# Kernel optimization log

Measured on AMD Instinct MI355X. Metric: run time of the kernel, lower is better.

Reference implementation:

```python
import jax, jax.numpy as jnp
import numpy as np

B, S, H = 4, 4096, 768
NB = 16            # n_blocks (first factor)
BSZ = H // NB      # 48, block size
LN_EPS = 1e-12


def setup_inputs() -> dict:
    key = jax.random.key(0)
    ks = jax.random.split(key, 6)
    hidden_states = jax.random.normal(ks[0], (B, S, H), dtype=jnp.float32)
    # Monarch factors: B1 has NB blocks of (BSZ,BSZ); B2 has BSZ blocks of (NB,NB)
    w1_blocks = jax.random.normal(ks[1], (NB, BSZ, BSZ), dtype=jnp.float32) / np.sqrt(BSZ)
    w2_blocks = jax.random.normal(ks[2], (BSZ, NB, NB), dtype=jnp.float32) / np.sqrt(NB)
    gate_w = jax.random.normal(ks[3], (H, H), dtype=jnp.float32) / np.sqrt(H)
    gate_b = jnp.zeros((H,), dtype=jnp.float32)
    out_w = jax.random.normal(ks[4], (H, H), dtype=jnp.float32) / np.sqrt(H)
    out_b = jnp.zeros((H,), dtype=jnp.float32)
    ln_gamma = jnp.ones((H,), dtype=jnp.float32)
    ln_beta = jnp.zeros((H,), dtype=jnp.float32)
    return {
        "hidden_states": hidden_states,
        "w1_blocks": w1_blocks,
        "w2_blocks": w2_blocks,
        "gate_w": gate_w,
        "gate_b": gate_b,
        "out_w": out_w,
        "out_b": out_b,
        "ln_gamma": ln_gamma,
        "ln_beta": ln_beta,
    }


def _monarch(x, w1, w2):
    # x: [B, S, H]; Monarch product P B2 P B1 applied to last dim.
    b, s, h = x.shape
    y = x.reshape(b, s, NB, BSZ)
    y = jnp.einsum('bski,kij->bskj', y, w1)      # block-diag (NB blocks of BSZxBSZ)
    y = jnp.swapaxes(y, -1, -2)                  # permute: [B,S,BSZ,NB]
    y = jnp.einsum('bsqi,qij->bsqj', y, w2)      # block-diag (BSZ blocks of NBxNB)
    y = jnp.swapaxes(y, -1, -2)                  # permute back: [B,S,NB,BSZ]
    return y.reshape(b, s, h)


def _layernorm(x, gamma, beta, eps):
    mu = jnp.mean(x, axis=-1, keepdims=True)
    var = jnp.mean(jnp.square(x - mu), axis=-1, keepdims=True)
    return (x - mu) * jax.lax.rsqrt(var + eps) * gamma + beta


def reference(hidden_states, w1_blocks, w2_blocks, gate_w, gate_b,
              out_w, out_b, ln_gamma, ln_beta):
    residual = hidden_states
    mixed = _monarch(hidden_states, w1_blocks, w2_blocks)
    gate = jax.nn.sigmoid(hidden_states @ gate_w.T + gate_b)
    h = mixed * gate
    h = h @ out_w.T + out_b
    # dropout is identity in eval / p=0
    return _layernorm(h + residual, ln_gamma, ln_beta, LN_EPS)
```

## Files before the change

kernel.cpp:

```cpp
#include <hip/hip_runtime.h>
#include <hip/hip_bf16.h>
#include <stdint.h>

#define HD 768

typedef __attribute__((ext_vector_type(8))) short bf16x8;
typedef __attribute__((ext_vector_type(4))) float f32x4;

typedef __attribute__((address_space(3))) void lds_void_t;
typedef const __attribute__((address_space(1))) void gbl_void_t;

__device__ inline void gload_lds16(const void* g, void* l) {
  __builtin_amdgcn_global_load_lds((gbl_void_t*)g, (lds_void_t*)l, 16, 0, 0);
}

__device__ inline unsigned short f2bf(float f) {
  union { float f; unsigned int u; } v; v.f = f;
  return (unsigned short)((v.u + 0x7fffu + ((v.u >> 16) & 1u)) >> 16);
}
__device__ inline float bf2f(unsigned short u) {
  union { unsigned int uu; float f; } v; v.uu = ((unsigned int)u) << 16;
  return v.f;
}

#define BAR() asm volatile("s_barrier" ::: "memory")
#define LGKM(N) { asm volatile("s_waitcnt lgkmcnt(" #N ")" ::: "memory"); __builtin_amdgcn_sched_barrier(0); }
#define VMC(N) asm volatile("s_waitcnt vmcnt(" #N ")" ::: "memory")

__global__ void prep_all_kernel(const float* __restrict__ x,
                                const float* __restrict__ gw, const float* __restrict__ ow,
                                const float* __restrict__ w1, const float* __restrict__ w2,
                                unsigned short* __restrict__ xb,
                                unsigned short* __restrict__ Gwb, unsigned short* __restrict__ Lwb,
                                unsigned short* __restrict__ Opk) {
  int bid = blockIdx.x;
  if (bid < 12288) {
    int i = bid * 256 + threadIdx.x;
    float4 v = ((const float4*)x)[i];
    ushort4 o;
    o.x = f2bf(v.x); o.y = f2bf(v.y); o.z = f2bf(v.z); o.w = f2bf(v.w);
    ((ushort4*)xb)[i] = o;
  } else if (bid < 14592) {
    int e = (bid - 12288) * 256 + threadIdx.x;
    Gwb[e] = f2bf(gw[e]);
  } else if (bid < 16896) {
    int e = (bid - 14592) * 256 + threadIdx.x;
    int n = e / 768, m = e - (e / 768) * 768;
    int k = n / 48, q = n - k * 48;
    int i2 = m / 48, ii = m - i2 * 48;
    float v = w1[(i2 * 48 + ii) * 48 + q] * w2[(q * 16 + i2) * 16 + k];
    Lwb[e] = f2bf(v);
  } else {
    int r = (bid - 16896) * 256 + threadIdx.x;
    int lane = r & 63;
    int ks = (r >> 6) % 24;
    int nt = r / (24 * 64);
    int n = nt * 16 + (lane & 15);
    int k = ks * 32 + (lane >> 4) * 8;
    bf16x8 pack;
#pragma unroll
    for (int j = 0; j < 8; ++j) pack[j] = (short)f2bf(ow[(size_t)n * HD + k + j]);
    *(bf16x8*)(Opk + (size_t)r * 8) = pack;
  }
}

__global__ __launch_bounds__(256, 2)
void gatemix_kernel(const unsigned short* __restrict__ xb,
                    const unsigned short* __restrict__ Gwb,
                    const unsigned short* __restrict__ Lwb,
                    const float* __restrict__ gate_b,
                    unsigned short* __restrict__ hb) {
  __shared__ __align__(16) unsigned char lds[81920];
  const int tid = threadIdx.x, lane = tid & 63;
  const int wid = tid >> 6, wm = wid >> 1, wn = wid & 1;
  const int lr = lane & 15, lg = lane >> 4;

  const int b = blockIdx.x;
  const int work = (b & 7) * 128 + (b >> 3);
  const int panel = work >> 3, nwin = work & 7;
  const size_t m0 = (size_t)panel * 128;
  const int n0 = nwin * 96;

  const int r0 = tid >> 3;
  const int sw = ((tid & 7) << 4) ^ ((r0 & 7) << 4);
  const int v0 = (0 * 32 + r0) * 1536 + sw;
  const int v1 = (1 * 32 + r0) * 1536 + sw;
  const int v2 = (2 * 32 + r0) * 1536 + sw;
  const int v3 = (3 * 32 + r0) * 1536 + sw;
  const unsigned char* aS = (const unsigned char*)xb + m0 * 1536;
  const unsigned char* gS = (const unsigned char*)Gwb + (size_t)n0 * 1536;
  const unsigned char* lS = (const unsigned char*)Lwb + (size_t)n0 * 1536;

#define STAGE_A(KT, BUF) { const unsigned char* s = aS + (KT) * 128; \
    gload_lds16(s + v0, lds + (BUF) * 16384 + tid * 16); \
    gload_lds16(s + v1, lds + (BUF) * 16384 + 4096 + tid * 16); \
    gload_lds16(s + v2, lds + (BUF) * 16384 + 8192 + tid * 16); \
    gload_lds16(s + v3, lds + (BUF) * 16384 + 12288 + tid * 16); }
#define STAGE_BG(KT, BUF) { const unsigned char* s = gS + (KT) * 128; \
    gload_lds16(s + v0, lds + 32768 + (BUF) * 12288 + tid * 16); \
    gload_lds16(s + v1, lds + 32768 + (BUF) * 12288 + 4096 + tid * 16); \
    gload_lds16(s + v2, lds + 32768 + (BUF) * 12288 + 8192 + tid * 16); }
#define STAGE_BL(KT, BUF) { const unsigned char* s = lS + (KT) * 128; \
    gload_lds16(s + v0, lds + 57344 + (BUF) * 12288 + tid * 16); \
    gload_lds16(s + v1, lds + 57344 + (BUF) * 12288 + 4096 + tid * 16); \
    gload_lds16(s + v2, lds + 57344 + (BUF) * 12288 + 8192 + tid * 16); }

  const int sx0 = (lg * 16) ^ ((lr & 7) << 4);
  const int sx1 = sx0 ^ 64;
  const unsigned char* baA0 = lds + (wm * 64 + lr) * 128 + sx0;
  const unsigned char* baA1 = lds + (wm * 64 + lr) * 128 + sx1;
  const unsigned char* baG0 = lds + 32768 + (wn * 48 + lr) * 128 + sx0;
  const unsigned char* baG1 = lds + 32768 + (wn * 48 + lr) * 128 + sx1;
  const unsigned char* baL0 = lds + 57344 + (wn * 48 + lr) * 128 + sx0;
  const unsigned char* baL1 = lds + 57344 + (wn * 48 + lr) * 128 + sx1;

  f32x4 accg[4][3], accm[4][3];
#pragma unroll
  for (int mt = 0; mt < 4; ++mt)
#pragma unroll
    for (int nt = 0; nt < 3; ++nt) { accg[mt][nt] = (f32x4){0,0,0,0}; accm[mt][nt] = (f32x4){0,0,0,0}; }

  bf16x8 aA[4], aB[4];
  bf16x8 bG[3], bL[3];

#define RD_AA(BUF) { _Pragma("unroll") for (int mt = 0; mt < 4; ++mt) \
      aA[mt] = *(const bf16x8*)(baA0 + (BUF) * 16384 + mt * 2048); }
#define RD_AB(BUF) { _Pragma("unroll") for (int mt = 0; mt < 4; ++mt) \
      aB[mt] = *(const bf16x8*)(baA1 + (BUF) * 16384 + mt * 2048); }
#define RD_BG0(BUF) { _Pragma("unroll") for (int nt = 0; nt < 3; ++nt) \
      bG[nt] = *(const bf16x8*)(baG0 + (BUF) * 12288 + nt * 2048); }
#define RD_BG1(BUF) { _Pragma("unroll") for (int nt = 0; nt < 3; ++nt) \
      bG[nt] = *(const bf16x8*)(baG1 + (BUF) * 12288 + nt * 2048); }
#define RD_BL0(BUF) { _Pragma("unroll") for (int nt = 0; nt < 3; ++nt) \
      bL[nt] = *(const bf16x8*)(baL0 + (BUF) * 12288 + nt * 2048); }
#define RD_BL1(BUF) { _Pragma("unroll") for (int nt = 0; nt < 3; ++nt) \
      bL[nt] = *(const bf16x8*)(baL1 + (BUF) * 12288 + nt * 2048); }
#define MM(ACC, AR, BR) { __builtin_amdgcn_s_setprio(1); \
    _Pragma("unroll") for (int mt = 0; mt < 4; ++mt) \
    _Pragma("unroll") for (int nt = 0; nt < 3; ++nt) \
      ACC[mt][nt] = __builtin_amdgcn_mfma_f32_16x16x32_bf16(AR[mt], BR[nt], ACC[mt][nt], 0, 0, 0); \
    __builtin_amdgcn_s_setprio(0); }

#define KT_BODY(KT, BUF, STG, VN) { \
    STAGE_BL((KT) + 1, (BUF) ^ 1); \
    RD_BL0(BUF); \
    LGKM(3); MM(accg, aA, bG); \
    RD_AB(BUF); RD_BG1(BUF); \
    LGKM(7); MM(accm, aA, bL); \
    RD_BL1(BUF); \
    LGKM(3); MM(accg, aB, bG); \
    BAR(); \
    if (STG) { STAGE_A((KT) + 2, BUF); STAGE_BG((KT) + 2, BUF); } \
    VMC(VN); \
    BAR(); \
    RD_AA((BUF) ^ 1); RD_BG0((BUF) ^ 1); \
    LGKM(7); MM(accm, aB, bL); }

  STAGE_A(0, 0); STAGE_BG(0, 0); STAGE_BL(0, 0); STAGE_A(1, 1); STAGE_BG(1, 1);
  VMC(7);
  BAR();
  RD_AA(0); RD_BG0(0);

#pragma unroll 1
  for (int kt = 0; kt < 10; kt += 2) {
    KT_BODY(kt, 0, 1, 7);
    KT_BODY(kt + 1, 1, 1, 7);
  }
  KT_BODY(10, 0, 0, 0);
  RD_BL0(1); LGKM(3); MM(accg, aA, bG);
  RD_AB(1); RD_BG1(1); LGKM(7); MM(accm, aA, bL);
  RD_BL1(1); LGKM(3); MM(accg, aB, bG);
  LGKM(0); MM(accm, aB, bL);

#pragma unroll
  for (int nt = 0; nt < 3; ++nt) {
    const int col = n0 + wn * 48 + nt * 16 + lr;
    const float gbv = gate_b[col];
#pragma unroll
    for (int mt = 0; mt < 4; ++mt) {
#pragma unroll
      for (int i = 0; i < 4; ++i) {
        float g = accg[mt][nt][i] + gbv;
        float s = 1.0f / (1.0f + __expf(-g));
        size_t row = m0 + wm * 64 + mt * 16 + lg * 4 + i;
        hb[row * 768 + col] = f2bf(s * accm[mt][nt][i]);
      }
    }
  }
#undef STAGE_A
#undef STAGE_BG
#undef STAGE_BL
#undef RD_AA
#undef RD_AB
#undef RD_BG0
#undef RD_BG1
#undef RD_BL0
#undef RD_BL1
#undef MM
#undef KT_BODY
}

__global__ __launch_bounds__(512, 2)
void out_ln_kernel(const unsigned short* __restrict__ hb,
                   const unsigned short* __restrict__ Opk,
                   const float* __restrict__ out_b,
                   const unsigned short* __restrict__ xb,
                   const float* __restrict__ gamma,
                   const float* __restrict__ beta,
                   float* __restrict__ out) {
  __shared__ __align__(16) unsigned char lds[16384];
  __shared__ float psum[64][8];
  __shared__ float psq[64][8];

  const int tid = threadIdx.x, lane = tid & 63, wid = tid >> 6;
  const int lr = lane & 15, lg = lane >> 4;
  const size_t m0 = (size_t)blockIdx.x * 64;

  const int srow = tid >> 3;
  const unsigned char* aSrc = (const unsigned char*)hb + (m0 + srow) * 1536
                              + (((tid & 7) << 4) ^ ((srow & 7) << 4));
#define STAGE_A(KT, BUF) gload_lds16(aSrc + (KT) * 128, lds + (BUF) * 8192 + tid * 16)

  const unsigned short* bBase = Opk + ((size_t)(wid * 6) * 24 * 64 + lane) * 8;
#define LOAD_B(KT, BR) { _Pragma("unroll") for (int nt = 0; nt < 6; ++nt) { \
      BR[nt * 2 + 0] = *(const bf16x8*)(bBase + nt * 12288 + ((KT) * 2 + 0) * 512); \
      BR[nt * 2 + 1] = *(const bf16x8*)(bBase + nt * 12288 + ((KT) * 2 + 1) * 512); } }

  const int sx0 = (lg * 16) ^ ((lr & 7) << 4);
  const unsigned char* baA0 = lds + lr * 128 + sx0;
  const unsigned char* baA1 = lds + lr * 128 + (sx0 ^ 64);
#define RD_A(BUF) { _Pragma("unroll") for (int mt = 0; mt < 4; ++mt) { \
      aF0[mt] = *(const bf16x8*)(baA0 + (BUF) * 8192 + mt * 2048); \
      aF1[mt] = *(const bf16x8*)(baA1 + (BUF) * 8192 + mt * 2048); } }

#define MM48(BR) { __builtin_amdgcn_s_setprio(1); \
    _Pragma("unroll") for (int mt = 0; mt < 4; ++mt) \
    _Pragma("unroll") for (int nt = 0; nt < 6; ++nt) { \
      acc[mt][nt] = __builtin_amdgcn_mfma_f32_16x16x32_bf16(aF0[mt], BR[nt * 2 + 0], acc[mt][nt], 0, 0, 0); \
      acc[mt][nt] = __builtin_amdgcn_mfma_f32_16x16x32_bf16(aF1[mt], BR[nt * 2 + 1], acc[mt][nt], 0, 0, 0); } \
    __builtin_amdgcn_s_setprio(0); }

  f32x4 acc[4][6];
#pragma unroll
  for (int mt = 0; mt < 4; ++mt)
#pragma unroll
    for (int nt = 0; nt < 6; ++nt) acc[mt][nt] = (f32x4){0, 0, 0, 0};

  bf16x8 aF0[4], aF1[4];
  bf16x8 bP[12], bQ[12];

#define KT_BODY(KT, BUF, BCUR, BNXT, LAST) { \
    if (!(LAST)) { STAGE_A((KT) + 1, (BUF) ^ 1); LOAD_B((KT) + 1, BNXT); } \
    RD_A(BUF); \
    LGKM(0); \
    if (!(LAST)) { VMC(13); } else { VMC(0); } \
    MM48(BCUR); \
    if (!(LAST)) { VMC(12); BAR(); } }

  STAGE_A(0, 0);
  LOAD_B(0, bP);
  VMC(12);
  BAR();

#pragma unroll 1
  for (int kt = 0; kt < 10; kt += 2) {
    KT_BODY(kt, 0, bP, bQ, 0);
    KT_BODY(kt + 1, 1, bQ, bP, 0);
  }
  KT_BODY(10, 0, bP, bQ, 0);
  KT_BODY(11, 1, bQ, bP, 1);

#pragma unroll
  for (int nt = 0; nt < 6; ++nt) {
    const int col = wid * 96 + nt * 16 + lr;
    const float obv = out_b[col];
#pragma unroll
    for (int mt = 0; mt < 4; ++mt) {
#pragma unroll
      for (int i = 0; i < 4; ++i) {
        size_t row = m0 + mt * 16 + lg * 4 + i;
        acc[mt][nt][i] += obv + bf2f(xb[row * 768 + col]);
      }
    }
  }
#pragma unroll
  for (int mt = 0; mt < 4; ++mt) {
#pragma unroll
    for (int i = 0; i < 4; ++i) {
      float s = 0.f, q = 0.f;
#pragma unroll
      for (int nt = 0; nt < 6; ++nt) { float v = acc[mt][nt][i]; s += v; q += v * v; }
#pragma unroll
      for (int off = 8; off >= 1; off >>= 1) {
        s += __shfl_xor(s, off);
        q += __shfl_xor(q, off);
      }
      if (lr == 0) {
        int rl = mt * 16 + lg * 4 + i;
        psum[rl][wid] = s; psq[rl][wid] = q;
      }
    }
  }
  __syncthreads();
#pragma unroll
  for (int mt = 0; mt < 4; ++mt) {
#pragma unroll
    for (int i = 0; i < 4; ++i) {
      int rl = mt * 16 + lg * 4 + i;
      float s = 0.f, q = 0.f;
#pragma unroll
      for (int w = 0; w < 8; ++w) { s += psum[rl][w]; q += psq[rl][w]; }
      float mu = s * (1.0f / 768.0f);
      float var = q * (1.0f / 768.0f) - mu * mu;
      var = var < 0.f ? 0.f : var;
      float rstd = rsqrtf(var + 1e-12f);
      size_t grow = m0 + rl;
#pragma unroll
      for (int nt = 0; nt < 6; ++nt) {
        int col = wid * 96 + nt * 16 + lr;
        out[grow * 768 + col] = (acc[mt][nt][i] - mu) * rstd * gamma[col] + beta[col];
      }
    }
  }
#undef STAGE_A
#undef LOAD_B
#undef RD_A
#undef MM48
#undef KT_BODY
}

extern "C" void kernel_launch(void* const* d_in, const int* in_sizes, int n_in,
                              void* d_out, int out_size, void* d_ws, size_t ws_size,
                              hipStream_t stream) {
  const float* x   = (const float*)d_in[0];
  const float* w1  = (const float*)d_in[1];
  const float* w2  = (const float*)d_in[2];
  const float* gw  = (const float*)d_in[3];
  const float* gb  = (const float*)d_in[4];
  const float* ow  = (const float*)d_in[5];
  const float* ob  = (const float*)d_in[6];
  const float* gam = (const float*)d_in[7];
  const float* bet = (const float*)d_in[8];
  float* out = (float*)d_out;

  char* ws = (char*)d_ws;
  unsigned short* xb  = (unsigned short*)(ws);
  unsigned short* hb  = (unsigned short*)(ws + 25165824);
  unsigned short* Gwb = (unsigned short*)(ws + 50331648);
  unsigned short* Lwb = (unsigned short*)(ws + 51511296);
  unsigned short* Opk = (unsigned short*)(ws + 52690944);

  prep_all_kernel<<<17184, 256, 0, stream>>>(x, gw, ow, w1, w2, xb, Gwb, Lwb, Opk);
  gatemix_kernel<<<1024, 256, 0, stream>>>(xb, Gwb, Lwb, gb, hb);
  out_ln_kernel<<<256, 512, 0, stream>>>(hb, Opk, ob, xb, gam, bet, out);
}
```

Before: 95.27 us.

## Fuse gate GEMM, factored Monarch mixing, out-proj and LayerNorm into one kernel

Replaces the three-kernel pipeline (x cast to bf16, a gate/Monarch GEMM writing an intermediate, then out-proj plus LayerNorm) with a small weight-prep kernel and a single fused kernel per 64-row tile. The fused kernel loads x once into LDS as bf16, runs the gate GEMM, applies the Monarch transform as two small block-diagonal MFMA stages through LDS scratch instead of a dense 768x768 product, writes the gated result back into the tile, then does the out-projection and LayerNorm. This removes the full-size bf16 x and h round-trips through global memory and about half the GEMM FLOPs. In exchange it uses about 150 KB of LDS per block with only 256 blocks, adds several barriers and serial phases, and the B operands come straight from global memory.

```diff
diff --git a/kernel.cpp b/kernel.cpp
--- a/kernel.cpp
+++ b/kernel.cpp
@@ -7,13 +7,6 @@
 typedef __attribute__((ext_vector_type(8))) short bf16x8;
 typedef __attribute__((ext_vector_type(4))) float f32x4;
 
-typedef __attribute__((address_space(3))) void lds_void_t;
-typedef const __attribute__((address_space(1))) void gbl_void_t;
-
-__device__ inline void gload_lds16(const void* g, void* l) {
-  __builtin_amdgcn_global_load_lds((gbl_void_t*)g, (lds_void_t*)l, 16, 0, 0);
-}
-
 __device__ inline unsigned short f2bf(float f) {
   union { float f; unsigned int u; } v; v.f = f;
   return (unsigned short)((v.u + 0x7fffu + ((v.u >> 16) & 1u)) >> 16);
@@ -23,35 +16,20 @@
   return v.f;
 }
 
-#define BAR() asm volatile("s_barrier" ::: "memory")
 #define LGKM(N) { asm volatile("s_waitcnt lgkmcnt(" #N ")" ::: "memory"); __builtin_amdgcn_sched_barrier(0); }
-#define VMC(N) asm volatile("s_waitcnt vmcnt(" #N ")" ::: "memory")
-
-__global__ void prep_all_kernel(const float* __restrict__ x,
-                                const float* __restrict__ gw, const float* __restrict__ ow,
-                                const float* __restrict__ w1, const float* __restrict__ w2,
-                                unsigned short* __restrict__ xb,
-                                unsigned short* __restrict__ Gwb, unsigned short* __restrict__ Lwb,
-                                unsigned short* __restrict__ Opk) {
+#define VMC(N) { asm volatile("s_waitcnt vmcnt(" #N ")" ::: "memory"); __builtin_amdgcn_sched_barrier(0); }
+
+__global__ void prep_kernel(const float* __restrict__ gw, const float* __restrict__ ow,
+                            const float* __restrict__ w1, const float* __restrict__ w2,
+                            unsigned short* __restrict__ Gpk,
+                            unsigned short* __restrict__ Opk,
+                            unsigned short* __restrict__ w1f,
+                            unsigned short* __restrict__ w2f) {
   int bid = blockIdx.x;
-  if (bid < 12288) {
-    int i = bid * 256 + threadIdx.x;
-    float4 v = ((const float4*)x)[i];
-    ushort4 o;
-    o.x = f2bf(v.x); o.y = f2bf(v.y); o.z = f2bf(v.z); o.w = f2bf(v.w);
-    ((ushort4*)xb)[i] = o;
-  } else if (bid < 14592) {
-    int e = (bid - 12288) * 256 + threadIdx.x;
-    Gwb[e] = f2bf(gw[e]);
-  } else if (bid < 16896) {
-    int e = (bid - 14592) * 256 + threadIdx.x;
-    int n = e / 768, m = e - (e / 768) * 768;
-    int k = n / 48, q = n - k * 48;
-    int i2 = m / 48, ii = m - i2 * 48;
-    float v = w1[(i2 * 48 + ii) * 48 + q] * w2[(q * 16 + i2) * 16 + k];
-    Lwb[e] = f2bf(v);
-  } else {
-    int r = (bid - 16896) * 256 + threadIdx.x;
+  if (bid < 576) {
+    const float* src = (bid < 288) ? gw : ow;
+    unsigned short* dst = (bid < 288) ? Gpk : Opk;
+    int r = ((bid < 288) ? bid : bid - 288) * 256 + threadIdx.x;
     int lane = r & 63;
     int ks = (r >> 6) % 24;
     int nt = r / (24 * 64);
@@ -59,156 +37,50 @@
     int k = ks * 32 + (lane >> 4) * 8;
     bf16x8 pack;
 #pragma unroll
-    for (int j = 0; j < 8; ++j) pack[j] = (short)f2bf(ow[(size_t)n * HD + k + j]);
-    *(bf16x8*)(Opk + (size_t)r * 8) = pack;
-  }
-}
-
-__global__ __launch_bounds__(256, 2)
-void gatemix_kernel(const unsigned short* __restrict__ xb,
-                    const unsigned short* __restrict__ Gwb,
-                    const unsigned short* __restrict__ Lwb,
-                    const float* __restrict__ gate_b,
-                    unsigned short* __restrict__ hb) {
-  __shared__ __align__(16) unsigned char lds[81920];
-  const int tid = threadIdx.x, lane = tid & 63;
-  const int wid = tid >> 6, wm = wid >> 1, wn = wid & 1;
-  const int lr = lane & 15, lg = lane >> 4;
-
-  const int b = blockIdx.x;
-  const int work = (b & 7) * 128 + (b >> 3);
-  const int panel = work >> 3, nwin = work & 7;
-  const size_t m0 = (size_t)panel * 128;
-  const int n0 = nwin * 96;
-
-  const int r0 = tid >> 3;
-  const int sw = ((tid & 7) << 4) ^ ((r0 & 7) << 4);
-  const int v0 = (0 * 32 + r0) * 1536 + sw;
-  const int v1 = (1 * 32 + r0) * 1536 + sw;
-  const int v2 = (2 * 32 + r0) * 1536 + sw;
-  const int v3 = (3 * 32 + r0) * 1536 + sw;
-  const unsigned char* aS = (const unsigned char*)xb + m0 * 1536;
-  const unsigned char* gS = (const unsigned char*)Gwb + (size_t)n0 * 1536;
-  const unsigned char* lS = (const unsigned char*)Lwb + (size_t)n0 * 1536;
-
-#define STAGE_A(KT, BUF) { const unsigned char* s = aS + (KT) * 128; \
-    gload_lds16(s + v0, lds + (BUF) * 16384 + tid * 16); \
-    gload_lds16(s + v1, lds + (BUF) * 16384 + 4096 + tid * 16); \
-    gload_lds16(s + v2, lds + (BUF) * 16384 + 8192 + tid * 16); \
-    gload_lds16(s + v3, lds + (BUF) * 16384 + 12288 + tid * 16); }
-#define STAGE_BG(KT, BUF) { const unsigned char* s = gS + (KT) * 128; \
-    gload_lds16(s + v0, lds + 32768 + (BUF) * 12288 + tid * 16); \
-    gload_lds16(s + v1, lds + 32768 + (BUF) * 12288 + 4096 + tid * 16); \
-    gload_lds16(s + v2, lds + 32768 + (BUF) * 12288 + 8192 + tid * 16); }
-#define STAGE_BL(KT, BUF) { const unsigned char* s = lS + (KT) * 128; \
-    gload_lds16(s + v0, lds + 57344 + (BUF) * 12288 + tid * 16); \
-    gload_lds16(s + v1, lds + 57344 + (BUF) * 12288 + 4096 + tid * 16); \
-    gload_lds16(s + v2, lds + 57344 + (BUF) * 12288 + 8192 + tid * 16); }
-
-  const int sx0 = (lg * 16) ^ ((lr & 7) << 4);
-  const int sx1 = sx0 ^ 64;
-  const unsigned char* baA0 = lds + (wm * 64 + lr) * 128 + sx0;
-  const unsigned char* baA1 = lds + (wm * 64 + lr) * 128 + sx1;
-  const unsigned char* baG0 = lds + 32768 + (wn * 48 + lr) * 128 + sx0;
-  const unsigned char* baG1 = lds + 32768 + (wn * 48 + lr) * 128 + sx1;
-  const unsigned char* baL0 = lds + 57344 + (wn * 48 + lr) * 128 + sx0;
-  const unsigned char* baL1 = lds + 57344 + (wn * 48 + lr) * 128 + sx1;
-
-  f32x4 accg[4][3], accm[4][3];
-#pragma unroll
-  for (int mt = 0; mt < 4; ++mt)
-#pragma unroll
-    for (int nt = 0; nt < 3; ++nt) { accg[mt][nt] = (f32x4){0,0,0,0}; accm[mt][nt] = (f32x4){0,0,0,0}; }
-
-  bf16x8 aA[4], aB[4];
-  bf16x8 bG[3], bL[3];
-
-#define RD_AA(BUF) { _Pragma("unroll") for (int mt = 0; mt < 4; ++mt) \
-      aA[mt] = *(const bf16x8*)(baA0 + (BUF) * 16384 + mt * 2048); }
-#define RD_AB(BUF) { _Pragma("unroll") for (int mt = 0; mt < 4; ++mt) \
-      aB[mt] = *(const bf16x8*)(baA1 + (BUF) * 16384 + mt * 2048); }
-#define RD_BG0(BUF) { _Pragma("unroll") for (int nt = 0; nt < 3; ++nt) \
-      bG[nt] = *(const bf16x8*)(baG0 + (BUF) * 12288 + nt * 2048); }
-#define RD_BG1(BUF) { _Pragma("unroll") for (int nt = 0; nt < 3; ++nt) \
-      bG[nt] = *(const bf16x8*)(baG1 + (BUF) * 12288 + nt * 2048); }
-#define RD_BL0(BUF) { _Pragma("unroll") for (int nt = 0; nt < 3; ++nt) \
-      bL[nt] = *(const bf16x8*)(baL0 + (BUF) * 12288 + nt * 2048); }
-#define RD_BL1(BUF) { _Pragma("unroll") for (int nt = 0; nt < 3; ++nt) \
-      bL[nt] = *(const bf16x8*)(baL1 + (BUF) * 12288 + nt * 2048); }
-#define MM(ACC, AR, BR) { __builtin_amdgcn_s_setprio(1); \
-    _Pragma("unroll") for (int mt = 0; mt < 4; ++mt) \
-    _Pragma("unroll") for (int nt = 0; nt < 3; ++nt) \
-      ACC[mt][nt] = __builtin_amdgcn_mfma_f32_16x16x32_bf16(AR[mt], BR[nt], ACC[mt][nt], 0, 0, 0); \
-    __builtin_amdgcn_s_setprio(0); }
-
-#define KT_BODY(KT, BUF, STG, VN) { \
-    STAGE_BL((KT) + 1, (BUF) ^ 1); \
-    RD_BL0(BUF); \
-    LGKM(3); MM(accg, aA, bG); \
-    RD_AB(BUF); RD_BG1(BUF); \
-    LGKM(7); MM(accm, aA, bL); \
-    RD_BL1(BUF); \
-    LGKM(3); MM(accg, aB, bG); \
-    BAR(); \
-    if (STG) { STAGE_A((KT) + 2, BUF); STAGE_BG((KT) + 2, BUF); } \
-    VMC(VN); \
-    BAR(); \
-    RD_AA((BUF) ^ 1); RD_BG0((BUF) ^ 1); \
-    LGKM(7); MM(accm, aB, bL); }
-
-  STAGE_A(0, 0); STAGE_BG(0, 0); STAGE_BL(0, 0); STAGE_A(1, 1); STAGE_BG(1, 1);
-  VMC(7);
-  BAR();
-  RD_AA(0); RD_BG0(0);
-
-#pragma unroll 1
-  for (int kt = 0; kt < 10; kt += 2) {
-    KT_BODY(kt, 0, 1, 7);
-    KT_BODY(kt + 1, 1, 1, 7);
-  }
-  KT_BODY(10, 0, 0, 0);
-  RD_BL0(1); LGKM(3); MM(accg, aA, bG);
-  RD_AB(1); RD_BG1(1); LGKM(7); MM(accm, aA, bL);
-  RD_BL1(1); LGKM(3); MM(accg, aB, bG);
-  LGKM(0); MM(accm, aB, bL);
-
-#pragma unroll
-  for (int nt = 0; nt < 3; ++nt) {
-    const int col = n0 + wn * 48 + nt * 16 + lr;
-    const float gbv = gate_b[col];
-#pragma unroll
-    for (int mt = 0; mt < 4; ++mt) {
-#pragma unroll
-      for (int i = 0; i < 4; ++i) {
-        float g = accg[mt][nt][i] + gbv;
-        float s = 1.0f / (1.0f + __expf(-g));
-        size_t row = m0 + wm * 64 + mt * 16 + lg * 4 + i;
-        hb[row * 768 + col] = f2bf(s * accm[mt][nt][i]);
-      }
-    }
-  }
-#undef STAGE_A
-#undef STAGE_BG
-#undef STAGE_BL
-#undef RD_AA
-#undef RD_AB
-#undef RD_BG0
-#undef RD_BG1
-#undef RD_BL0
-#undef RD_BL1
-#undef MM
-#undef KT_BODY
+    for (int j = 0; j < 8; ++j) pack[j] = (short)f2bf(src[(size_t)n * HD + k + j]);
+    *(bf16x8*)(dst + (size_t)r * 8) = pack;
+  } else if (bid < 600) {
+    int e = (bid - 576) * 256 + threadIdx.x;
+    int lane = e & 63, fi = e >> 6;
+    int ks = fi & 1, nt = (fi >> 1) % 3, k = fi / 6;
+    int lrr = lane & 15, lgg = lane >> 4;
+    int q = nt * 16 + lrr;
+    bf16x8 pack;
+#pragma unroll
+    for (int j = 0; j < 8; ++j) {
+      int kk = ks * 32 + lgg * 8 + j;
+      float v = (kk < 48) ? w1[(k * 48 + kk) * 48 + q] : 0.0f;
+      pack[j] = (short)f2bf(v);
+    }
+    *(bf16x8*)(w1f + (size_t)e * 8) = pack;
+  } else {
+    int e = (bid - 600) * 256 + threadIdx.x;
+    int lane = e & 63, q = e >> 6;
+    int lrr = lane & 15, lgg = lane >> 4;
+    bf16x8 pack;
+#pragma unroll
+    for (int j = 0; j < 8; ++j) {
+      int kk = lgg * 8 + j;
+      float v = (kk < 16) ? w2[(q * 16 + kk) * 16 + lrr] : 0.0f;
+      pack[j] = (short)f2bf(v);
+    }
+    *(bf16x8*)(w2f + (size_t)e * 8) = pack;
+  }
 }
 
 __global__ __launch_bounds__(512, 2)
-void out_ln_kernel(const unsigned short* __restrict__ hb,
-                   const unsigned short* __restrict__ Opk,
-                   const float* __restrict__ out_b,
-                   const unsigned short* __restrict__ xb,
-                   const float* __restrict__ gamma,
-                   const float* __restrict__ beta,
-                   float* __restrict__ out) {
-  __shared__ __align__(16) unsigned char lds[16384];
+void fused_kernel(const float* __restrict__ x,
+                  const unsigned short* __restrict__ Gpk,
+                  const unsigned short* __restrict__ Opk,
+                  const unsigned short* __restrict__ w1f,
+                  const unsigned short* __restrict__ w2f,
+                  const float* __restrict__ gate_b,
+                  const float* __restrict__ out_b,
+                  const float* __restrict__ gamma,
+                  const float* __restrict__ beta,
+                  float* __restrict__ out) {
+  __shared__ __align__(16) unsigned char tile[98304];
+  __shared__ __align__(16) unsigned char scratch[49152];
   __shared__ float psum[64][8];
   __shared__ float psq[64][8];
 
@@ -216,80 +88,152 @@
   const int lr = lane & 15, lg = lane >> 4;
   const size_t m0 = (size_t)blockIdx.x * 64;
 
-  const int srow = tid >> 3;
-  const unsigned char* aSrc = (const unsigned char*)hb + (m0 + srow) * 1536
-                              + (((tid & 7) << 4) ^ ((srow & 7) << 4));
-#define STAGE_A(KT, BUF) gload_lds16(aSrc + (KT) * 128, lds + (BUF) * 8192 + tid * 16)
-
-  const unsigned short* bBase = Opk + ((size_t)(wid * 6) * 24 * 64 + lane) * 8;
-#define LOAD_B(KT, BR) { _Pragma("unroll") for (int nt = 0; nt < 6; ++nt) { \
-      BR[nt * 2 + 0] = *(const bf16x8*)(bBase + nt * 12288 + ((KT) * 2 + 0) * 512); \
-      BR[nt * 2 + 1] = *(const bf16x8*)(bBase + nt * 12288 + ((KT) * 2 + 1) * 512); } }
+  float gbv[6], obv[6];
+#pragma unroll
+  for (int nt = 0; nt < 6; ++nt) {
+    int col = wid * 96 + nt * 16 + lr;
+    gbv[nt] = gate_b[col];
+    obv[nt] = out_b[col];
+  }
+
+  {
+    const float4* xs = (const float4*)x + m0 * 192;
+#pragma unroll
+    for (int p = 0; p < 24; ++p) {
+      int id = p * 512 + tid;
+      float4 v = xs[id];
+      int row = id / 192, c4 = id - row * 192;
+      uint2 u;
+      u.x = (unsigned int)f2bf(v.x) | ((unsigned int)f2bf(v.y) << 16);
+      u.y = (unsigned int)f2bf(v.z) | ((unsigned int)f2bf(v.w) << 16);
+      *(uint2*)(tile + row * 1536 + ((c4 * 8) ^ ((row & 7) << 4))) = u;
+    }
+  }
+  __syncthreads();
 
   const int sx0 = (lg * 16) ^ ((lr & 7) << 4);
-  const unsigned char* baA0 = lds + lr * 128 + sx0;
-  const unsigned char* baA1 = lds + lr * 128 + (sx0 ^ 64);
-#define RD_A(BUF) { _Pragma("unroll") for (int mt = 0; mt < 4; ++mt) { \
-      aF0[mt] = *(const bf16x8*)(baA0 + (BUF) * 8192 + mt * 2048); \
-      aF1[mt] = *(const bf16x8*)(baA1 + (BUF) * 8192 + mt * 2048); } }
-
-#define MM48(BR) { __builtin_amdgcn_s_setprio(1); \
+  const unsigned char* baA0 = tile + lr * 1536 + sx0;
+  const unsigned char* baA1 = tile + lr * 1536 + (sx0 ^ 64);
+  const unsigned short* gB = Gpk + ((size_t)(wid * 6) * 24 * 64 + lane) * 8;
+  const unsigned short* oB = Opk + ((size_t)(wid * 6) * 24 * 64 + lane) * 8;
+
+  bf16x8 aF0[4], aF1[4];
+  bf16x8 bP[12], bQ[12];
+
+#define LOAD_B(BB, KT, BR) { _Pragma("unroll") for (int nt = 0; nt < 6; ++nt) { \
+      BR[nt * 2 + 0] = *(const bf16x8*)((BB) + nt * 12288 + ((KT) * 2 + 0) * 512); \
+      BR[nt * 2 + 1] = *(const bf16x8*)((BB) + nt * 12288 + ((KT) * 2 + 1) * 512); } }
+#define RD_A(KT) { _Pragma("unroll") for (int mt = 0; mt < 4; ++mt) { \
+      aF0[mt] = *(const bf16x8*)(baA0 + mt * 24576 + (KT) * 128); \
+      aF1[mt] = *(const bf16x8*)(baA1 + mt * 24576 + (KT) * 128); } }
+#define MM48(ACC, BR) { __builtin_amdgcn_s_setprio(1); \
     _Pragma("unroll") for (int mt = 0; mt < 4; ++mt) \
     _Pragma("unroll") for (int nt = 0; nt < 6; ++nt) { \
-      acc[mt][nt] = __builtin_amdgcn_mfma_f32_16x16x32_bf16(aF0[mt], BR[nt * 2 + 0], acc[mt][nt], 0, 0, 0); \
-      acc[mt][nt] = __builtin_amdgcn_mfma_f32_16x16x32_bf16(aF1[mt], BR[nt * 2 + 1], acc[mt][nt], 0, 0, 0); } \
+      ACC[mt][nt] = __builtin_amdgcn_mfma_f32_16x16x32_bf16(aF0[mt], BR[nt * 2 + 0], ACC[mt][nt], 0, 0, 0); \
+      ACC[mt][nt] = __builtin_amdgcn_mfma_f32_16x16x32_bf16(aF1[mt], BR[nt * 2 + 1], ACC[mt][nt], 0, 0, 0); } \
     __builtin_amdgcn_s_setprio(0); }
-
-  f32x4 acc[4][6];
+#define GEMM_LOOP(BB, ACC) { \
+    LOAD_B(BB, 0, bP); \
+    _Pragma("unroll 1") \
+    for (int kt = 0; kt < 10; kt += 2) { \
+      LOAD_B(BB, kt + 1, bQ); RD_A(kt); LGKM(0); VMC(12); MM48(ACC, bP); \
+      LOAD_B(BB, kt + 2, bP); RD_A(kt + 1); LGKM(0); VMC(12); MM48(ACC, bQ); \
+    } \
+    LOAD_B(BB, 11, bQ); RD_A(10); LGKM(0); VMC(12); MM48(ACC, bP); \
+    RD_A(11); LGKM(0); VMC(0); MM48(ACC, bQ); }
+
+  f32x4 accG[4][6];
 #pragma unroll
   for (int mt = 0; mt < 4; ++mt)
 #pragma unroll
-    for (int nt = 0; nt < 6; ++nt) acc[mt][nt] = (f32x4){0, 0, 0, 0};
-
-  bf16x8 aF0[4], aF1[4];
-  bf16x8 bP[12], bQ[12];
-
-#define KT_BODY(KT, BUF, BCUR, BNXT, LAST) { \
-    if (!(LAST)) { STAGE_A((KT) + 1, (BUF) ^ 1); LOAD_B((KT) + 1, BNXT); } \
-    RD_A(BUF); \
-    LGKM(0); \
-    if (!(LAST)) { VMC(13); } else { VMC(0); } \
-    MM48(BCUR); \
-    if (!(LAST)) { VMC(12); BAR(); } }
-
-  STAGE_A(0, 0);
-  LOAD_B(0, bP);
-  VMC(12);
-  BAR();
-
-#pragma unroll 1
-  for (int kt = 0; kt < 10; kt += 2) {
-    KT_BODY(kt, 0, bP, bQ, 0);
-    KT_BODY(kt + 1, 1, bQ, bP, 0);
-  }
-  KT_BODY(10, 0, bP, bQ, 0);
-  KT_BODY(11, 1, bQ, bP, 1);
-
-#pragma unroll
-  for (int nt = 0; nt < 6; ++nt) {
-    const int col = wid * 96 + nt * 16 + lr;
-    const float obv = out_b[col];
-#pragma unroll
-    for (int mt = 0; mt < 4; ++mt) {
-#pragma unroll
-      for (int i = 0; i < 4; ++i) {
-        size_t row = m0 + mt * 16 + lg * 4 + i;
-        acc[mt][nt][i] += obv + bf2f(xb[row * 768 + col]);
-      }
-    }
-  }
+    for (int nt = 0; nt < 6; ++nt) accG[mt][nt] = (f32x4){0, 0, 0, 0};
+  GEMM_LOOP(gB, accG);
+
+  f32x4 accO[4][6];
+
+#define MONARCH_HALF(H) { \
+     \
+    _Pragma("unroll") for (int kb = 0; kb < 2; ++kb) { \
+      const int k = wid * 2 + kb; \
+      const unsigned short* wf = w1f + (size_t)(k * 6) * 512 + lane * 8; \
+      bf16x8 w1b0 = *(const bf16x8*)(wf + 0 * 512); \
+      bf16x8 w1b1 = *(const bf16x8*)(wf + 1 * 512); \
+      bf16x8 w1b2 = *(const bf16x8*)(wf + 2 * 512); \
+      bf16x8 w1b3 = *(const bf16x8*)(wf + 3 * 512); \
+      bf16x8 w1b4 = *(const bf16x8*)(wf + 4 * 512); \
+      bf16x8 w1b5 = *(const bf16x8*)(wf + 5 * 512); \
+      _Pragma("unroll") for (int mtl = 0; mtl < 2; ++mtl) { \
+        const int row = (H) * 32 + mtl * 16 + lr; \
+        const int rsw = (lr & 7) << 4; \
+        bf16x8 a0 = *(const bf16x8*)(tile + row * 1536 + ((k * 96 + lg * 16) ^ rsw)); \
+        bf16x8 a1 = (bf16x8){0, 0, 0, 0, 0, 0, 0, 0}; \
+        if (lg < 2) a1 = *(const bf16x8*)(tile + row * 1536 + ((k * 96 + 64 + lg * 16) ^ rsw)); \
+        f32x4 c0 = {0,0,0,0}, c1 = {0,0,0,0}, c2 = {0,0,0,0}; \
+        c0 = __builtin_amdgcn_mfma_f32_16x16x32_bf16(a0, w1b0, c0, 0, 0, 0); \
+        c0 = __builtin_amdgcn_mfma_f32_16x16x32_bf16(a1, w1b1, c0, 0, 0, 0); \
+        c1 = __builtin_amdgcn_mfma_f32_16x16x32_bf16(a0, w1b2, c1, 0, 0, 0); \
+        c1 = __builtin_amdgcn_mfma_f32_16x16x32_bf16(a1, w1b3, c1, 0, 0, 0); \
+        c2 = __builtin_amdgcn_mfma_f32_16x16x32_bf16(a0, w1b4, c2, 0, 0, 0); \
+        c2 = __builtin_amdgcn_mfma_f32_16x16x32_bf16(a1, w1b5, c2, 0, 0, 0); \
+        _Pragma("unroll") for (int i = 0; i < 4; ++i) { \
+          int rl = mtl * 16 + lg * 4 + i; \
+          int zsw = (rl & 7) << 4; \
+          *(unsigned short*)(scratch + ((rl * 1536 + 0 * 512 + lr * 32 + k * 2) ^ zsw)) = f2bf(c0[i]); \
+          *(unsigned short*)(scratch + ((rl * 1536 + 1 * 512 + lr * 32 + k * 2) ^ zsw)) = f2bf(c1[i]); \
+          *(unsigned short*)(scratch + ((rl * 1536 + 2 * 512 + lr * 32 + k * 2) ^ zsw)) = f2bf(c2[i]); } } } \
+    __syncthreads(); \
+     \
+    { unsigned int upk[2][4][3]; \
+    _Pragma("unroll") for (int qq = 0; qq < 6; ++qq) { \
+      const int q = wid * 6 + qq; \
+      bf16x8 bw = *(const bf16x8*)(w2f + (size_t)q * 512 + lane * 8); \
+      _Pragma("unroll") for (int mtl = 0; mtl < 2; ++mtl) { \
+        int rl = mtl * 16 + lr; \
+        bf16x8 a = (bf16x8){0, 0, 0, 0, 0, 0, 0, 0}; \
+        if (lg < 2) a = *(const bf16x8*)(scratch + ((rl * 1536 + q * 32 + lg * 16) ^ ((rl & 7) << 4))); \
+        f32x4 c = {0, 0, 0, 0}; \
+        c = __builtin_amdgcn_mfma_f32_16x16x32_bf16(a, bw, c, 0, 0, 0); \
+        _Pragma("unroll") for (int i = 0; i < 4; ++i) { \
+          unsigned int h = (unsigned int)f2bf(c[i]); \
+          if (qq & 1) upk[mtl][i][qq >> 1] |= (h << 16); \
+          else        upk[mtl][i][qq >> 1] = h; } } } \
+    __syncthreads();   \
+     \
+    _Pragma("unroll") for (int mtl = 0; mtl < 2; ++mtl) \
+    _Pragma("unroll") for (int i = 0; i < 4; ++i) { \
+      int rl = mtl * 16 + lg * 4 + i; \
+      int base = rl * 1536 + lr * 96 + wid * 12; \
+      int msw = (rl & 7) << 4; \
+      _Pragma("unroll") for (int p = 0; p < 3; ++p) \
+        *(unsigned int*)(scratch + ((base + p * 4) ^ msw)) = upk[mtl][i][p]; } } \
+    __syncthreads(); \
+     \
+    _Pragma("unroll") for (int mtl = 0; mtl < 2; ++mtl) \
+    _Pragma("unroll") for (int nt = 0; nt < 6; ++nt) \
+    _Pragma("unroll") for (int i = 0; i < 4; ++i) { \
+      int rl = mtl * 16 + lg * 4 + i; \
+      int row = (H) * 32 + rl; \
+      int colb = (wid * 96 + nt * 16 + lr) * 2; \
+      float mval = bf2f(*(const unsigned short*)(scratch + ((rl * 1536 + colb) ^ ((rl & 7) << 4)))); \
+      float g = accG[(H) * 2 + mtl][nt][i] + gbv[nt]; \
+      float s = 1.0f / (1.0f + __expf(-g)); \
+      unsigned char* tp = tile + row * 1536 + (colb ^ ((row & 7) << 4)); \
+      accO[(H) * 2 + mtl][nt][i] = bf2f(*(const unsigned short*)tp) + obv[nt]; \
+      *(unsigned short*)tp = f2bf(s * mval); } \
+    __syncthreads(); }
+
+  MONARCH_HALF(0)
+  MONARCH_HALF(1)
+
+  GEMM_LOOP(oB, accO);
+
 #pragma unroll
   for (int mt = 0; mt < 4; ++mt) {
 #pragma unroll
     for (int i = 0; i < 4; ++i) {
       float s = 0.f, q = 0.f;
 #pragma unroll
-      for (int nt = 0; nt < 6; ++nt) { float v = acc[mt][nt][i]; s += v; q += v * v; }
+      for (int nt = 0; nt < 6; ++nt) { float v = accO[mt][nt][i]; s += v; q += v * v; }
 #pragma unroll
       for (int off = 8; off >= 1; off >>= 1) {
         s += __shfl_xor(s, off);
@@ -318,15 +262,15 @@
 #pragma unroll
       for (int nt = 0; nt < 6; ++nt) {
         int col = wid * 96 + nt * 16 + lr;
-        out[grow * 768 + col] = (acc[mt][nt][i] - mu) * rstd * gamma[col] + beta[col];
+        out[grow * 768 + col] = (accO[mt][nt][i] - mu) * rstd * gamma[col] + beta[col];
       }
     }
   }
-#undef STAGE_A
 #undef LOAD_B
 #undef RD_A
 #undef MM48
-#undef KT_BODY
+#undef GEMM_LOOP
+#undef MONARCH_HALF
 }
 
 extern "C" void kernel_launch(void* const* d_in, const int* in_sizes, int n_in,
@@ -344,13 +288,11 @@
   float* out = (float*)d_out;
 
   char* ws = (char*)d_ws;
-  unsigned short* xb  = (unsigned short*)(ws);
-  unsigned short* hb  = (unsigned short*)(ws + 25165824);
-  unsigned short* Gwb = (unsigned short*)(ws + 50331648);
-  unsigned short* Lwb = (unsigned short*)(ws + 51511296);
-  unsigned short* Opk = (unsigned short*)(ws + 52690944);
-
-  prep_all_kernel<<<17184, 256, 0, stream>>>(x, gw, ow, w1, w2, xb, Gwb, Lwb, Opk);
-  gatemix_kernel<<<1024, 256, 0, stream>>>(xb, Gwb, Lwb, gb, hb);
-  out_ln_kernel<<<256, 512, 0, stream>>>(hb, Opk, ob, xb, gam, bet, out);
-}
+  unsigned short* Gpk = (unsigned short*)(ws);
+  unsigned short* Opk = (unsigned short*)(ws + 1179648);
+  unsigned short* w1f = (unsigned short*)(ws + 2359296);
+  unsigned short* w2f = (unsigned short*)(ws + 2457600);
+
+  prep_kernel<<<612, 256, 0, stream>>>(gw, ow, w1, w2, Gpk, Opk, w1f, w2f);
+  fused_kernel<<<256, 512, 0, stream>>>(x, Gpk, Opk, w1f, w2f, gb, ob, gam, bet, out);
+}
```

Result: slower. 102.8 us (+7.9%).
